# Performance work log

Measured on AMD Instinct MI355X. Metric: run time of the kernel, lower is better.

Reference implementation:

```python
import jax, jax.numpy as jnp
import numpy as np

B, N, HID, E, H = 4, 256, 256, 64, 4
OUT = HID // 2          # 128
D = OUT // H            # 32
AGG = H * (2 * D + 1)   # 260 = concat(mean D, attn_sum 1, max D) per head


def setup_inputs() -> dict:
    key = jax.random.key(0)
    ks = jax.random.split(key, 7)
    s = 0.05
    return {
        "h_x": jax.random.normal(ks[0], (B, N, HID), jnp.float32),
        "h_e": jax.random.normal(ks[1], (B, N, N, E), jnp.float32),
        "h_m": jnp.ones((B, N), jnp.float32),
        "W_Q": jax.random.normal(ks[2], (OUT, HID), jnp.float32) * s,
        "W_K": jax.random.normal(ks[3], (OUT, E), jnp.float32) * s,
        "W_V": jax.random.normal(ks[4], (OUT, E), jnp.float32) * s,
        "W_R": jax.random.normal(ks[5], (OUT, AGG), jnp.float32) * s,
    }


def reference(h_x, h_e, h_m, W_Q, W_K, W_V, W_R):
    # queries from node features: [B,H,N,D]
    h_q = (h_x @ W_Q.T).reshape(B, N, H, D).transpose(0, 2, 1, 3)
    # keys/values from dense pairwise edge features: [B,H,N,N,D]
    h_k = jnp.einsum('bnme,ce->bnmc', h_e, W_K).reshape(B, N, N, H, D).transpose(0, 3, 1, 2, 4)
    h_v = jnp.einsum('bnme,ce->bnmc', h_e, W_V).reshape(B, N, N, H, D).transpose(0, 3, 1, 2, 4)
    # broadcast dot: [B,H,N,N]
    scores = jnp.einsum('bhnd,bhnmd->bhnm', h_q, h_k) / np.float32(np.sqrt(D))
    # per-node mask broadcast as [B,1,N,1] (masks query rows)
    scores = jnp.where(h_m[:, None, :, None] == 0, -jnp.inf, scores)
    # NOTE: original code softmaxes over dim=1 = HEAD axis (faithful)
    attn = jax.nn.softmax(scores, axis=1)                      # [B,H,N,N]
    attn_w = attn[..., None] * h_v                             # [B,H,N,N,D]
    aggr_sum = attn_w.sum(axis=3)                              # [B,H,N,D]
    attn_sum = attn.sum(axis=3, keepdims=True) + 1e-8          # [B,H,N,1]
    aggr_mean = aggr_sum / attn_sum
    aggr_max = attn_w.max(axis=3)                              # [B,H,N,D]
    multi = jnp.concatenate([aggr_mean, attn_sum, aggr_max], axis=-1)  # [B,H,N,2D+1]
    aggr_out = multi.transpose(0, 2, 1, 3).reshape(B, N, AGG)  # [B,N,260]
    return aggr_out @ W_R.T                                    # [B,N,OUT]
```

## Files before the change

### kernel.cpp

```cpp
#include <hip/hip_runtime.h>

constexpr int Bb   = 4;
constexpr int Nn   = 256;
constexpr int HID  = 256;
constexpr int Ee   = 64;
constexpr int Hh   = 4;
constexpr int OUTc = 128;
constexpr int Dd   = 32;
constexpr int AGG  = 260;
constexpr int REC  = 264;
constexpr int QA_LD = 264;

constexpr size_t WS_QBUF  = 0;
constexpr size_t WS_WRT   = WS_QBUF + (size_t)Bb * Nn * OUTc;
constexpr size_t WS_FRAGV = WS_WRT + (size_t)AGG * OUTc;
constexpr size_t WS_FRAGQ = WS_FRAGV + 4096;
constexpr size_t WS_UFRAG = WS_FRAGQ + 16384;

typedef __attribute__((ext_vector_type(8))) short short8;
typedef __attribute__((ext_vector_type(4))) float floatx4;

__device__ __forceinline__ unsigned short f2bf(float f) {
    union { float f; unsigned u; } x; x.f = f;
    unsigned r = x.u + 0x7FFFu + ((x.u >> 16) & 1u);
    return (unsigned short)(r >> 16);
}

__device__ __forceinline__ short8 pack8(floatx4 f0, floatx4 f1) {
    short8 v;
    v[0] = (short)f2bf(f0[0]); v[1] = (short)f2bf(f0[1]);
    v[2] = (short)f2bf(f0[2]); v[3] = (short)f2bf(f0[3]);
    v[4] = (short)f2bf(f1[0]); v[5] = (short)f2bf(f1[1]);
    v[6] = (short)f2bf(f1[2]); v[7] = (short)f2bf(f1[3]);
    return v;
}

__global__ __launch_bounds__(256)
void eama_pack(const float* __restrict__ W_Q, const float* __restrict__ W_V,
               const float* __restrict__ W_R,
               unsigned short* __restrict__ wfragV, unsigned short* __restrict__ wfragQ,
               float* __restrict__ W_RT)
{
    const int tid = threadIdx.x;
    const int bid = blockIdx.x;

    if (bid < 4) {
        const int e    = bid * 256 + tid;
        const int lane = e & 63;
        const int ks   = (e >> 6) & 1;
        const int ct   = e >> 7;
        const int ncol = lane & 15, q8 = lane >> 4;
        const float* row = W_V + (ct * 16 + ncol) * Ee;
        const int k0 = ks * 32 + q8 * 8;
        floatx4 f0 = *(const floatx4*)(row + k0);
        floatx4 f1 = *(const floatx4*)(row + k0 + 4);
        *(short8*)(wfragV + (size_t)e * 8) = pack8(f0, f1);
    } else if (bid < 20) {
        const int e    = (bid - 4) * 256 + tid;
        const int lane = e & 63;
        const int ks   = (e >> 6) & 7;
        const int ct   = (e >> 9) & 1;
        const int wv   = (e >> 10) & 3;
        const int ncol = lane & 15, q8 = lane >> 4;
        const float* row = W_Q + (wv * 32 + ct * 16 + ncol) * HID;
        const int k0 = ks * 32 + q8 * 8;
        floatx4 f0 = *(const floatx4*)(row + k0);
        floatx4 f1 = *(const floatx4*)(row + k0 + 4);
        *(short8*)(wfragQ + (size_t)e * 8) = pack8(f0, f1);
    } else {
        const int i = (bid - 20) * 256 + tid;
        if (i < AGG * OUTc) {
            const int c = i & 127, j = i >> 7;
            W_RT[j * OUTc + c] = W_R[c * AGG + j];
        }
    }
}

__global__ __launch_bounds__(256)
void eama_qproj(const float* __restrict__ h_x, const unsigned short* __restrict__ wfragQ,
                float* __restrict__ qbuf)
{
    __shared__ __align__(16) unsigned short sA[16 * QA_LD];
    const int tid  = threadIdx.x;
    const int b0   = blockIdx.x * 16;
    const int lane = tid & 63;
    const int wv   = tid >> 6;
    const int ncol = lane & 15, q8 = lane >> 4;

    short8 bq[2][8];
    #pragma unroll
    for (int ct = 0; ct < 2; ++ct)
        #pragma unroll
        for (int ks = 0; ks < 8; ++ks) {
            const int e = ((wv * 2 + ct) * 8 + ks) * 64 + lane;
            bq[ct][ks] = *(const short8*)(wfragQ + (size_t)e * 8);
        }
    #pragma unroll
    for (int i = 0; i < 2; ++i) {
        const int idx = tid + i * 256;
        const int r = idx >> 5, blk = idx & 31;
        const float* src = h_x + (size_t)(b0 + r) * HID + blk * 8;
        floatx4 f0 = *(const floatx4*)(src);
        floatx4 f1 = *(const floatx4*)(src + 4);
        *(short8*)&sA[r * QA_LD + blk * 8] = pack8(f0, f1);
    }
    __syncthreads();
    floatx4 acc[2] = {(floatx4){0,0,0,0}, (floatx4){0,0,0,0}};
    #pragma unroll
    for (int ks = 0; ks < 8; ++ks) {
        short8 a = *(const short8*)&sA[ncol * QA_LD + ks * 32 + q8 * 8];
        acc[0] = __builtin_amdgcn_mfma_f32_16x16x32_bf16(a, bq[0][ks], acc[0], 0, 0, 0);
        acc[1] = __builtin_amdgcn_mfma_f32_16x16x32_bf16(a, bq[1][ks], acc[1], 0, 0, 0);
    }
    #pragma unroll
    for (int ct = 0; ct < 2; ++ct)
        #pragma unroll
        for (int rr = 0; rr < 4; ++rr)
            qbuf[(size_t)(b0 + q8 * 4 + rr) * OUTc + wv * 32 + ct * 16 + ncol] = acc[ct][rr];
}

__global__ __launch_bounds__(256)
void eama_u(const float* __restrict__ qbuf, const float* __restrict__ W_K,
            unsigned short* __restrict__ ufrag)
{
    __shared__ float sq[OUTc];
    __shared__ __align__(16) float sU[Hh][Ee];
    const int tid = threadIdx.x;
    const int bn  = blockIdx.x;
    if (tid < OUTc) sq[tid] = qbuf[bn * OUTc + tid];
    __syncthreads();
    {
        const int h = tid >> 6, e = tid & 63;
        float a0 = 0.f, a1 = 0.f;
        #pragma unroll
        for (int d = 0; d < Dd; d += 2) {
            a0 = fmaf(sq[h * Dd + d],     W_K[(h * Dd + d) * Ee + e],     a0);
            a1 = fmaf(sq[h * Dd + d + 1], W_K[(h * Dd + d + 1) * Ee + e], a1);
        }
        sU[h][e] = (a0 + a1) * 0.1767766952966369f;
    }
    __syncthreads();
    if (tid < 128) {
        const int ks = tid >> 6, l = tid & 63;
        const int nc = l & 15, q8 = l >> 4;
        short8 v = {0,0,0,0,0,0,0,0};
        if (nc < Hh) {
            const float* u = &sU[nc][ks * 32 + q8 * 8];
            floatx4 f0 = *(const floatx4*)u;
            floatx4 f1 = *(const floatx4*)(u + 4);
            v = pack8(f0, f1);
        }
        *(short8*)(ufrag + ((size_t)(bn * 2 + ks) * 64 + l) * 8) = v;
    }
}

__global__ __launch_bounds__(512, 1)
void eama_main(const float* __restrict__ h_e, const float* __restrict__ h_m,
               const unsigned short* __restrict__ wfragV,
               const unsigned short* __restrict__ ufrag,
               const float* __restrict__ W_RT, float* __restrict__ out)
{
    __shared__ float sVS[8][OUTc];
    __shared__ float sVM[8][OUTc];
    __shared__ float sAS[8][Hh];
    __shared__ float sAsum[Hh];
    __shared__ __align__(16) float sM[REC];
    __shared__ float sAcc[4][OUTc];

    const int tid  = threadIdx.x;
    const int lane = tid & 63;
    const int w    = tid >> 6;
    const int ncol = lane & 15;
    const int bn   = blockIdx.x;
    const float maskv = h_m[bn];

    short8 bfV[8][2];
    #pragma unroll
    for (int ct = 0; ct < 8; ++ct)
        #pragma unroll
        for (int ks = 0; ks < 2; ++ks)
            bfV[ct][ks] = *(const short8*)(wfragV + ((size_t)(ct * 2 + ks) * 64 + lane) * 8);
    short8 bu[2];
    bu[0] = *(const short8*)(ufrag + ((size_t)(bn * 2 + 0) * 64 + lane) * 8);
    bu[1] = *(const short8*)(ufrag + ((size_t)(bn * 2 + 1) * 64 + lane) * 8);

    float vs[8], vm[8], asum = 0.f;
    #pragma unroll
    for (int ct = 0; ct < 8; ++ct) { vs[ct] = 0.f; vm[ct] = -3.402823466e38f; }

    const float* heb = h_e + (size_t)bn * Nn * Ee;
    const int q8 = lane >> 4;

    #pragma unroll
    for (int it = 0; it < 2; ++it) {
        const int m0 = w * 32 + it * 16;
        const float* ar = heb + (size_t)(m0 + ncol) * Ee;
        short8 af[2];
        #pragma unroll
        for (int ks = 0; ks < 2; ++ks) {
            floatx4 f0 = *(const floatx4*)(ar + ks * 32 + q8 * 8);
            floatx4 f1 = *(const floatx4*)(ar + ks * 32 + q8 * 8 + 4);
            af[ks] = pack8(f0, f1);
        }
        floatx4 accV[8], accS = (floatx4){0,0,0,0};
        #pragma unroll
        for (int ct = 0; ct < 8; ++ct) accV[ct] = (floatx4){0,0,0,0};
        #pragma unroll
        for (int ks = 0; ks < 2; ++ks) {
            #pragma unroll
            for (int ct = 0; ct < 8; ++ct)
                accV[ct] = __builtin_amdgcn_mfma_f32_16x16x32_bf16(af[ks], bfV[ct][ks], accV[ct], 0, 0, 0);
            accS = __builtin_amdgcn_mfma_f32_16x16x32_bf16(af[ks], bu[ks], accS, 0, 0, 0);
        }
        float a[4];
        #pragma unroll
        for (int r = 0; r < 4; ++r) {
            float s = (maskv != 0.f) ? accS[r] : -1e30f;
            float m1 = fmaxf(s, __shfl_xor(s, 1, 64));
            m1 = fmaxf(m1, __shfl_xor(m1, 2, 64));
            float e = __expf(s - m1);
            float t = e + __shfl_xor(e, 1, 64);
            t += __shfl_xor(t, 2, 64);
            a[r] = e / t;
        }
        asum += a[0] + a[1] + a[2] + a[3];
        #pragma unroll
        for (int h = 0; h < Hh; ++h) {
            const int src = (lane & 48) | h;
            float aw0 = __shfl(a[0], src, 64);
            float aw1 = __shfl(a[1], src, 64);
            float aw2 = __shfl(a[2], src, 64);
            float aw3 = __shfl(a[3], src, 64);
            #pragma unroll
            for (int g = 0; g < 2; ++g) {
                const int ct = h * 2 + g;
                float p0 = aw0 * accV[ct][0];
                float p1 = aw1 * accV[ct][1];
                float p2 = aw2 * accV[ct][2];
                float p3 = aw3 * accV[ct][3];
                vs[ct] += (p0 + p1) + (p2 + p3);
                vm[ct] = fmaxf(vm[ct], fmaxf(fmaxf(p0, p1), fmaxf(p2, p3)));
            }
        }
    }

    #pragma unroll
    for (int ct = 0; ct < 8; ++ct) {
        vs[ct] += __shfl_xor(vs[ct], 16, 64);
        vs[ct] += __shfl_xor(vs[ct], 32, 64);
        vm[ct] = fmaxf(vm[ct], __shfl_xor(vm[ct], 16, 64));
        vm[ct] = fmaxf(vm[ct], __shfl_xor(vm[ct], 32, 64));
    }
    asum += __shfl_xor(asum, 16, 64);
    asum += __shfl_xor(asum, 32, 64);

    if (lane < 16) {
        #pragma unroll
        for (int ct = 0; ct < 8; ++ct) {
            sVS[w][ct * 16 + lane] = vs[ct];
            sVM[w][ct * 16 + lane] = vm[ct];
        }
    }
    if (lane < Hh) sAS[w][lane] = asum;
    __syncthreads();
    if (tid < Hh) {
        float a = 1e-8f;
        #pragma unroll
        for (int ww = 0; ww < 8; ++ww) a += sAS[ww][tid];
        sAsum[tid] = a;
    }
    __syncthreads();
    if (tid < OUTc) {
        float vsum = 0.f, vmax = -3.402823466e38f;
        #pragma unroll
        for (int ww = 0; ww < 8; ++ww) {
            vsum += sVS[ww][tid];
            vmax = fmaxf(vmax, sVM[ww][tid]);
        }
        const int h = tid >> 5, d = tid & 31;
        sM[h * 65 + d]      = vsum / sAsum[h];
        sM[h * 65 + 33 + d] = vmax;
        if (tid < Hh) sM[tid * 65 + 32] = sAsum[tid];
    }
    __syncthreads();
    {
        const int c = tid & 127, part = tid >> 7;
        const int j0 = part * 65;
        float acc = 0.f;
        #pragma unroll 5
        for (int j = j0; j < j0 + 65; ++j)
            acc = fmaf(sM[j], W_RT[j * OUTc + c], acc);
        sAcc[part][c] = acc;
    }
    __syncthreads();
    if (tid < OUTc)
        out[bn * OUTc + tid] = (sAcc[0][tid] + sAcc[1][tid]) + (sAcc[2][tid] + sAcc[3][tid]);
}

extern "C" void kernel_launch(void* const* d_in, const int* in_sizes, int n_in,
                              void* d_out, int out_size, void* d_ws, size_t ws_size,
                              hipStream_t stream) {
    const float* h_x = (const float*)d_in[0];
    const float* h_e = (const float*)d_in[1];
    const float* h_m = (const float*)d_in[2];
    const float* W_Q = (const float*)d_in[3];
    const float* W_K = (const float*)d_in[4];
    const float* W_V = (const float*)d_in[5];
    const float* W_R = (const float*)d_in[6];
    float* out = (float*)d_out;

    float* ws            = (float*)d_ws;
    float* qbuf          = ws + WS_QBUF;
    float* W_RT          = ws + WS_WRT;
    unsigned short* wfV  = (unsigned short*)(ws + WS_FRAGV);
    unsigned short* wfQ  = (unsigned short*)(ws + WS_FRAGQ);
    unsigned short* ufr  = (unsigned short*)(ws + WS_UFRAG);

    eama_pack<<<dim3(150), dim3(256), 0, stream>>>(W_Q, W_V, W_R, wfV, wfQ, W_RT);
    eama_qproj<<<dim3(Bb * Nn / 16), dim3(256), 0, stream>>>(h_x, wfQ, qbuf);
    eama_u<<<dim3(Bb * Nn), dim3(256), 0, stream>>>(qbuf, W_K, ufr);
    eama_main<<<dim3(Bb * Nn), dim3(512), 0, stream>>>(h_e, h_m, wfV, ufr, W_RT, out);
}
```

Measured before the change: 139.8 us.

## Fuse Q projection with U computation and split main kernel over key slices

Merges the query projection and the per-node U = q·W_K kernels into one, so q no longer round-trips through global memory. The main kernel is split across four key slices per node with 256-thread blocks. Softmax over heads now goes through shared-memory score tiles instead of lane shuffles, and V fragments are loaded inside the loop rather than held in registers. Partial sums, maxes and attention sums go to a workspace and are reduced, along with the W_R projection, in a new stage-2 kernel. This adds parallelism and occupancy for the h_e streaming, at the cost of an extra launch and a partials round-trip.

```diff
diff --git a/kernel.cpp b/kernel.cpp
--- a/kernel.cpp
+++ b/kernel.cpp
@@ -9,10 +9,11 @@
 constexpr int Dd   = 32;
 constexpr int AGG  = 260;
 constexpr int REC  = 264;
+constexpr int NSL  = 4;
 constexpr int QA_LD = 264;
 
-constexpr size_t WS_QBUF  = 0;
-constexpr size_t WS_WRT   = WS_QBUF + (size_t)Bb * Nn * OUTc;
+constexpr size_t WS_WSP   = 0;
+constexpr size_t WS_WRT   = WS_WSP + (size_t)Bb * Nn * NSL * REC;
 constexpr size_t WS_FRAGV = WS_WRT + (size_t)AGG * OUTc;
 constexpr size_t WS_FRAGQ = WS_FRAGV + 4096;
 constexpr size_t WS_UFRAG = WS_FRAGQ + 16384;
@@ -77,10 +78,12 @@
 }
 
 __global__ __launch_bounds__(256)
-void eama_qproj(const float* __restrict__ h_x, const unsigned short* __restrict__ wfragQ,
-                float* __restrict__ qbuf)
+void eama_qu(const float* __restrict__ h_x, const unsigned short* __restrict__ wfragQ,
+             const float* __restrict__ W_K, unsigned short* __restrict__ ufrag)
 {
     __shared__ __align__(16) unsigned short sA[16 * QA_LD];
+    __shared__ __align__(16) float sqL[16][132];
+    __shared__ __align__(16) float sU2[16][256];
     const int tid  = threadIdx.x;
     const int b0   = blockIdx.x * 16;
     const int lane = tid & 63;
@@ -116,132 +119,125 @@
     for (int ct = 0; ct < 2; ++ct)
         #pragma unroll
         for (int rr = 0; rr < 4; ++rr)
-            qbuf[(size_t)(b0 + q8 * 4 + rr) * OUTc + wv * 32 + ct * 16 + ncol] = acc[ct][rr];
-}
-
-__global__ __launch_bounds__(256)
-void eama_u(const float* __restrict__ qbuf, const float* __restrict__ W_K,
-            unsigned short* __restrict__ ufrag)
-{
-    __shared__ float sq[OUTc];
-    __shared__ __align__(16) float sU[Hh][Ee];
-    const int tid = threadIdx.x;
-    const int bn  = blockIdx.x;
-    if (tid < OUTc) sq[tid] = qbuf[bn * OUTc + tid];
-    __syncthreads();
+            sqL[q8 * 4 + rr][wv * 32 + ct * 16 + ncol] = acc[ct][rr];
+    __syncthreads();
+
     {
-        const int h = tid >> 6, e = tid & 63;
-        float a0 = 0.f, a1 = 0.f;
-        #pragma unroll
-        for (int d = 0; d < Dd; d += 2) {
-            a0 = fmaf(sq[h * Dd + d],     W_K[(h * Dd + d) * Ee + e],     a0);
-            a1 = fmaf(sq[h * Dd + d + 1], W_K[(h * Dd + d + 1) * Ee + e], a1);
-        }
-        sU[h][e] = (a0 + a1) * 0.1767766952966369f;
-    }
-    __syncthreads();
-    if (tid < 128) {
-        const int ks = tid >> 6, l = tid & 63;
-        const int nc = l & 15, q8 = l >> 4;
-        short8 v = {0,0,0,0,0,0,0,0};
+        const int h = wv, e = lane;
+        float a16[16];
+        #pragma unroll
+        for (int i = 0; i < 16; ++i) a16[i] = 0.f;
+        #pragma unroll
+        for (int d4 = 0; d4 < 8; ++d4) {
+            float wk0 = W_K[(h * Dd + d4 * 4 + 0) * Ee + e];
+            float wk1 = W_K[(h * Dd + d4 * 4 + 1) * Ee + e];
+            float wk2 = W_K[(h * Dd + d4 * 4 + 2) * Ee + e];
+            float wk3 = W_K[(h * Dd + d4 * 4 + 3) * Ee + e];
+            #pragma unroll
+            for (int b16 = 0; b16 < 16; ++b16) {
+                floatx4 qv = *(const floatx4*)&sqL[b16][h * Dd + d4 * 4];
+                a16[b16] += (qv[0] * wk0 + qv[1] * wk1) + (qv[2] * wk2 + qv[3] * wk3);
+            }
+        }
+        #pragma unroll
+        for (int b16 = 0; b16 < 16; ++b16)
+            sU2[b16][h * 64 + e] = a16[b16] * 0.1767766952966369f;
+    }
+    __syncthreads();
+
+    #pragma unroll
+    for (int k = 0; k < 8; ++k) {
+        const int ei   = tid + k * 256;
+        const int b16  = ei >> 7;
+        const int rest = ei & 127;
+        const int ks   = rest >> 6;
+        const int l    = rest & 63;
+        const int nc   = l & 15, qq = l >> 4;
+        short8 v = {0, 0, 0, 0, 0, 0, 0, 0};
         if (nc < Hh) {
-            const float* u = &sU[nc][ks * 32 + q8 * 8];
-            floatx4 f0 = *(const floatx4*)u;
-            floatx4 f1 = *(const floatx4*)(u + 4);
+            floatx4 f0 = *(const floatx4*)&sU2[b16][nc * 64 + ks * 32 + qq * 8];
+            floatx4 f1 = *(const floatx4*)&sU2[b16][nc * 64 + ks * 32 + qq * 8 + 4];
             v = pack8(f0, f1);
         }
-        *(short8*)(ufrag + ((size_t)(bn * 2 + ks) * 64 + l) * 8) = v;
-    }
-}
-
-__global__ __launch_bounds__(512, 1)
+        *(short8*)(ufrag + ((size_t)((b0 + b16) * 2 + ks) * 64 + l) * 8) = v;
+    }
+}
+
+__global__ __launch_bounds__(256, 4)
 void eama_main(const float* __restrict__ h_e, const float* __restrict__ h_m,
                const unsigned short* __restrict__ wfragV,
                const unsigned short* __restrict__ ufrag,
-               const float* __restrict__ W_RT, float* __restrict__ out)
+               float* __restrict__ wsP)
 {
-    __shared__ float sVS[8][OUTc];
-    __shared__ float sVM[8][OUTc];
-    __shared__ float sAS[8][Hh];
-    __shared__ float sAsum[Hh];
-    __shared__ __align__(16) float sM[REC];
-    __shared__ float sAcc[4][OUTc];
+    __shared__ __align__(16) float sS[4][16][4];
+    __shared__ float sVS[4][OUTc];
+    __shared__ float sVM[4][OUTc];
+    __shared__ float sAS[4][Hh];
 
     const int tid  = threadIdx.x;
     const int lane = tid & 63;
     const int w    = tid >> 6;
     const int ncol = lane & 15;
+    const int q8   = lane >> 4;
     const int bn   = blockIdx.x;
+    const int sl   = blockIdx.y;
     const float maskv = h_m[bn];
 
-    short8 bfV[8][2];
-    #pragma unroll
-    for (int ct = 0; ct < 8; ++ct)
-        #pragma unroll
-        for (int ks = 0; ks < 2; ++ks)
-            bfV[ct][ks] = *(const short8*)(wfragV + ((size_t)(ct * 2 + ks) * 64 + lane) * 8);
-    short8 bu[2];
-    bu[0] = *(const short8*)(ufrag + ((size_t)(bn * 2 + 0) * 64 + lane) * 8);
-    bu[1] = *(const short8*)(ufrag + ((size_t)(bn * 2 + 1) * 64 + lane) * 8);
-
-    float vs[8], vm[8], asum = 0.f;
+    const int m0 = sl * 64 + w * 16;
+    const float* ar = h_e + ((size_t)bn * Nn + m0 + ncol) * Ee;
+
+    floatx4 a00 = *(const floatx4*)(ar + q8 * 8);
+    floatx4 a01 = *(const floatx4*)(ar + q8 * 8 + 4);
+    floatx4 a10 = *(const floatx4*)(ar + 32 + q8 * 8);
+    floatx4 a11 = *(const floatx4*)(ar + 32 + q8 * 8 + 4);
+    short8 bu0 = *(const short8*)(ufrag + ((size_t)(bn * 2 + 0) * 64 + lane) * 8);
+    short8 bu1 = *(const short8*)(ufrag + ((size_t)(bn * 2 + 1) * 64 + lane) * 8);
+
+    short8 af0 = pack8(a00, a01);
+    short8 af1 = pack8(a10, a11);
+
+    floatx4 accV[8], accS = (floatx4){0, 0, 0, 0};
+    #pragma unroll
+    for (int ct = 0; ct < 8; ++ct) accV[ct] = (floatx4){0, 0, 0, 0};
+
+    #pragma unroll
+    for (int ct = 0; ct < 8; ++ct) {
+        short8 bf0 = *(const short8*)(wfragV + ((size_t)(ct * 2 + 0) * 64 + lane) * 8);
+        short8 bf1 = *(const short8*)(wfragV + ((size_t)(ct * 2 + 1) * 64 + lane) * 8);
+        accV[ct] = __builtin_amdgcn_mfma_f32_16x16x32_bf16(af0, bf0, accV[ct], 0, 0, 0);
+        accV[ct] = __builtin_amdgcn_mfma_f32_16x16x32_bf16(af1, bf1, accV[ct], 0, 0, 0);
+    }
+    accS = __builtin_amdgcn_mfma_f32_16x16x32_bf16(af0, bu0, accS, 0, 0, 0);
+    accS = __builtin_amdgcn_mfma_f32_16x16x32_bf16(af1, bu1, accS, 0, 0, 0);
+
+    if (ncol < Hh) {
+        #pragma unroll
+        for (int r = 0; r < 4; ++r)
+            sS[w][q8 * 4 + r][ncol] = (maskv != 0.f) ? accS[r] : -1e30f;
+    }
+    __syncthreads();
+
+    float vs[8], vm[8], asumH = 0.f;
     #pragma unroll
     for (int ct = 0; ct < 8; ++ct) { vs[ct] = 0.f; vm[ct] = -3.402823466e38f; }
-
-    const float* heb = h_e + (size_t)bn * Nn * Ee;
-    const int q8 = lane >> 4;
-
-    #pragma unroll
-    for (int it = 0; it < 2; ++it) {
-        const int m0 = w * 32 + it * 16;
-        const float* ar = heb + (size_t)(m0 + ncol) * Ee;
-        short8 af[2];
-        #pragma unroll
-        for (int ks = 0; ks < 2; ++ks) {
-            floatx4 f0 = *(const floatx4*)(ar + ks * 32 + q8 * 8);
-            floatx4 f1 = *(const floatx4*)(ar + ks * 32 + q8 * 8 + 4);
-            af[ks] = pack8(f0, f1);
-        }
-        floatx4 accV[8], accS = (floatx4){0,0,0,0};
-        #pragma unroll
-        for (int ct = 0; ct < 8; ++ct) accV[ct] = (floatx4){0,0,0,0};
-        #pragma unroll
-        for (int ks = 0; ks < 2; ++ks) {
-            #pragma unroll
-            for (int ct = 0; ct < 8; ++ct)
-                accV[ct] = __builtin_amdgcn_mfma_f32_16x16x32_bf16(af[ks], bfV[ct][ks], accV[ct], 0, 0, 0);
-            accS = __builtin_amdgcn_mfma_f32_16x16x32_bf16(af[ks], bu[ks], accS, 0, 0, 0);
-        }
-        float a[4];
-        #pragma unroll
-        for (int r = 0; r < 4; ++r) {
-            float s = (maskv != 0.f) ? accS[r] : -1e30f;
-            float m1 = fmaxf(s, __shfl_xor(s, 1, 64));
-            m1 = fmaxf(m1, __shfl_xor(m1, 2, 64));
-            float e = __expf(s - m1);
-            float t = e + __shfl_xor(e, 1, 64);
-            t += __shfl_xor(t, 2, 64);
-            a[r] = e / t;
-        }
-        asum += a[0] + a[1] + a[2] + a[3];
-        #pragma unroll
-        for (int h = 0; h < Hh; ++h) {
-            const int src = (lane & 48) | h;
-            float aw0 = __shfl(a[0], src, 64);
-            float aw1 = __shfl(a[1], src, 64);
-            float aw2 = __shfl(a[2], src, 64);
-            float aw3 = __shfl(a[3], src, 64);
-            #pragma unroll
-            for (int g = 0; g < 2; ++g) {
-                const int ct = h * 2 + g;
-                float p0 = aw0 * accV[ct][0];
-                float p1 = aw1 * accV[ct][1];
-                float p2 = aw2 * accV[ct][2];
-                float p3 = aw3 * accV[ct][3];
-                vs[ct] += (p0 + p1) + (p2 + p3);
-                vm[ct] = fmaxf(vm[ct], fmaxf(fmaxf(p0, p1), fmaxf(p2, p3)));
-            }
-        }
+    #pragma unroll
+    for (int r = 0; r < 4; ++r) {
+        floatx4 sc = *(const floatx4*)&sS[w][q8 * 4 + r][0];
+        float mx = fmaxf(fmaxf(sc[0], sc[1]), fmaxf(sc[2], sc[3]));
+        float e0 = __expf(sc[0] - mx), e1 = __expf(sc[1] - mx);
+        float e2 = __expf(sc[2] - mx), e3 = __expf(sc[3] - mx);
+        float inv = 1.f / ((e0 + e1) + (e2 + e3));
+        float a0 = e0 * inv, a1 = e1 * inv, a2 = e2 * inv, a3 = e3 * inv;
+        asumH += (ncol & 2) ? ((ncol & 1) ? a3 : a2) : ((ncol & 1) ? a1 : a0);
+        float p;
+        p = a0 * accV[0][r]; vs[0] += p; vm[0] = fmaxf(vm[0], p);
+        p = a0 * accV[1][r]; vs[1] += p; vm[1] = fmaxf(vm[1], p);
+        p = a1 * accV[2][r]; vs[2] += p; vm[2] = fmaxf(vm[2], p);
+        p = a1 * accV[3][r]; vs[3] += p; vm[3] = fmaxf(vm[3], p);
+        p = a2 * accV[4][r]; vs[4] += p; vm[4] = fmaxf(vm[4], p);
+        p = a2 * accV[5][r]; vs[5] += p; vm[5] = fmaxf(vm[5], p);
+        p = a3 * accV[6][r]; vs[6] += p; vm[6] = fmaxf(vm[6], p);
+        p = a3 * accV[7][r]; vs[7] += p; vm[7] = fmaxf(vm[7], p);
     }
 
     #pragma unroll
@@ -251,8 +247,8 @@
         vm[ct] = fmaxf(vm[ct], __shfl_xor(vm[ct], 16, 64));
         vm[ct] = fmaxf(vm[ct], __shfl_xor(vm[ct], 32, 64));
     }
-    asum += __shfl_xor(asum, 16, 64);
-    asum += __shfl_xor(asum, 32, 64);
+    asumH += __shfl_xor(asumH, 16, 64);
+    asumH += __shfl_xor(asumH, 32, 64);
 
     if (lane < 16) {
         #pragma unroll
@@ -261,40 +257,65 @@
             sVM[w][ct * 16 + lane] = vm[ct];
         }
     }
-    if (lane < Hh) sAS[w][lane] = asum;
-    __syncthreads();
+    if (lane < Hh) sAS[w][lane] = asumH;
+    __syncthreads();
+    if (tid < OUTc) {
+        const size_t base = (size_t)(bn * NSL + sl) * REC;
+        float vsum = (sVS[0][tid] + sVS[1][tid]) + (sVS[2][tid] + sVS[3][tid]);
+        float vmax = fmaxf(fmaxf(sVM[0][tid], sVM[1][tid]), fmaxf(sVM[2][tid], sVM[3][tid]));
+        wsP[base + tid]        = vsum;
+        wsP[base + OUTc + tid] = vmax;
+        if (tid < Hh)
+            wsP[base + 2 * OUTc + tid] =
+                (sAS[0][tid] + sAS[1][tid]) + (sAS[2][tid] + sAS[3][tid]);
+    }
+}
+
+__global__ __launch_bounds__(256)
+void eama_stage2(const float* __restrict__ wsP, const float* __restrict__ W_RT,
+                 float* __restrict__ out)
+{
+    __shared__ __align__(16) float sM[REC];
+    __shared__ float sAs[Hh];
+    __shared__ float sAcc[2][OUTc];
+    const int tid = threadIdx.x;
+    const int bn  = blockIdx.x;
+    const size_t base = (size_t)bn * NSL * REC;
+
+    float vsum = 0.f, vmax = -3.402823466e38f;
+    if (tid < OUTc) {
+        #pragma unroll
+        for (int tp = 0; tp < NSL; ++tp) {
+            vsum += wsP[base + tp * REC + tid];
+            vmax = fmaxf(vmax, wsP[base + tp * REC + OUTc + tid]);
+        }
+    }
     if (tid < Hh) {
         float a = 1e-8f;
         #pragma unroll
-        for (int ww = 0; ww < 8; ++ww) a += sAS[ww][tid];
-        sAsum[tid] = a;
+        for (int tp = 0; tp < NSL; ++tp) a += wsP[base + tp * REC + 2 * OUTc + tid];
+        sAs[tid] = a;
     }
     __syncthreads();
     if (tid < OUTc) {
-        float vsum = 0.f, vmax = -3.402823466e38f;
-        #pragma unroll
-        for (int ww = 0; ww < 8; ++ww) {
-            vsum += sVS[ww][tid];
-            vmax = fmaxf(vmax, sVM[ww][tid]);
-        }
         const int h = tid >> 5, d = tid & 31;
-        sM[h * 65 + d]      = vsum / sAsum[h];
+        sM[h * 65 + d]      = vsum / sAs[h];
         sM[h * 65 + 33 + d] = vmax;
-        if (tid < Hh) sM[tid * 65 + 32] = sAsum[tid];
+        if (tid < Hh) sM[tid * 65 + 32] = sAs[tid];
     }
     __syncthreads();
     {
         const int c = tid & 127, part = tid >> 7;
-        const int j0 = part * 65;
+        const int j0 = part * 130;
         float acc = 0.f;
         #pragma unroll 5
-        for (int j = j0; j < j0 + 65; ++j)
+        for (int j = j0; j < j0 + 130; ++j)
             acc = fmaf(sM[j], W_RT[j * OUTc + c], acc);
         sAcc[part][c] = acc;
     }
     __syncthreads();
     if (tid < OUTc)
-        out[bn * OUTc + tid] = (sAcc[0][tid] + sAcc[1][tid]) + (sAcc[2][tid] + sAcc[3][tid]);
+        out[bn * OUTc + tid] = sAcc[0][tid] + sAcc[1][tid];
 }
 
 extern "C" void kernel_launch(void* const* d_in, const int* in_sizes, int n_in,
@@ -310,14 +331,14 @@
     float* out = (float*)d_out;
 
     float* ws            = (float*)d_ws;
-    float* qbuf          = ws + WS_QBUF;
+    float* wsP           = ws + WS_WSP;
     float* W_RT          = ws + WS_WRT;
     unsigned short* wfV  = (unsigned short*)(ws + WS_FRAGV);
     unsigned short* wfQ  = (unsigned short*)(ws + WS_FRAGQ);
     unsigned short* ufr  = (unsigned short*)(ws + WS_UFRAG);
 
     eama_pack<<<dim3(150), dim3(256), 0, stream>>>(W_Q, W_V, W_R, wfV, wfQ, W_RT);
-    eama_qproj<<<dim3(Bb * Nn / 16), dim3(256), 0, stream>>>(h_x, wfQ, qbuf);
-    eama_u<<<dim3(Bb * Nn), dim3(256), 0, stream>>>(qbuf, W_K, ufr);
-    eama_main<<<dim3(Bb * Nn), dim3(512), 0, stream>>>(h_e, h_m, wfV, ufr, W_RT, out);
-}
+    eama_qu<<<dim3(Bb * Nn / 16), dim3(256), 0, stream>>>(h_x, wfQ, W_K, ufr);
+    eama_main<<<dim3(Bb * Nn, NSL), dim3(256), 0, stream>>>(h_e, h_m, wfV, ufr, wsP);
+    eama_stage2<<<dim3(Bb * Nn), dim3(256), 0, stream>>>(wsP, W_RT, out);
+}
```

After: 135.0 us. 1.04x faster.
